# Kernel optimization log

Measured on AMD Instinct MI355X. Metric: run time of the kernel, lower is better.

The kernel has to match this reference:

```python
import jax, jax.numpy as jnp
import numpy as np

NUM_ENTS = 100000
NUM_RELS = 237
IN_CH, OUT_CH, KER = 1, 32, 9
IN_DIM = 200
K = 10
OUT_DIM = K * IN_DIM                      # 2000
L_IN = OUT_DIM // IN_CH                   # 2000
L_OUT = (L_IN - KER) // 1 + 1             # 1992
FC_LEN = OUT_CH * L_OUT                   # 63744
BATCH = 512
EPS = 1e-5


def _bn(x, gamma, beta, axes):
    # training-mode batch norm (biased variance), matching torch BatchNorm1d forward
    m = jnp.mean(x, axis=axes, keepdims=True)
    v = jnp.var(x, axis=axes, keepdims=True)
    return (x - m) * jax.lax.rsqrt(v + EPS) * gamma + beta


def setup_inputs() -> dict:
    key = jax.random.key(0)
    ks = jax.random.split(key, 8)
    xavier = lambda k, shape, fan: jax.random.normal(k, shape, jnp.float32) * np.sqrt(2.0 / fan)
    E = xavier(ks[0], (NUM_ENTS, IN_DIM), NUM_ENTS + IN_DIM)
    R = xavier(ks[1], (NUM_RELS * 2, OUT_CH, IN_CH, KER), OUT_CH * IN_CH * KER)
    e_W = xavier(ks[2], (IN_DIM, OUT_DIM), IN_DIM + OUT_DIM)
    fc_W = xavier(ks[3], (IN_DIM, FC_LEN), IN_DIM + FC_LEN)  # torch Linear weight [out, in]
    return {
        "E": E, "R": R, "e_W": e_W, "fc_W": fc_W,
        "bn0_gamma": jnp.ones((IN_DIM,), jnp.float32), "bn0_beta": jnp.zeros((IN_DIM,), jnp.float32),
        "bn1_gamma": jnp.ones((OUT_CH,), jnp.float32), "bn1_beta": jnp.zeros((OUT_CH,), jnp.float32),
        "bn2_gamma": jnp.ones((IN_DIM,), jnp.float32), "bn2_beta": jnp.zeros((IN_DIM,), jnp.float32),
        "e1_idx": jax.random.randint(ks[4], (BATCH,), 0, NUM_ENTS),
        "r_idx": jax.random.randint(ks[5], (BATCH,), 0, NUM_RELS * 2),
    }


def reference(E, R, e_W, fc_W, bn0_gamma, bn0_beta, bn1_gamma, bn1_beta,
              bn2_gamma, bn2_beta, e1_idx, r_idx):
    B = e1_idx.shape[0]
    x = E[e1_idx]                                   # [B, 200]
    x = _bn(x, bn0_gamma, bn0_beta, axes=0)
    x = x @ e_W                                     # [B, 2000]
    k = R[r_idx]                                    # [B, O, C, KER] per-sample filters
    x = x.reshape(B, IN_CH, L_IN)                   # [B, C, L_in]
    # per-sample grouped conv1d == batched small matmul over sliding windows
    win = jnp.arange(L_OUT)[:, None] + jnp.arange(KER)[None, :]  # [L_out, KER]
    patches = x[:, :, win]                          # [B, C, L_out, KER]
    x = jnp.einsum('bock,bclk->bol', k, patches)    # [B, O, L_out]
    x = _bn(x, bn1_gamma[:, None], bn1_beta[:, None], axes=(0, 2))
    x = x.reshape(B, FC_LEN)
    x = x @ fc_W.T                                  # [B, 200]
    x = jnp.tanh(_bn(x, bn2_gamma, bn2_beta, axes=0))
    logits = x @ E.T                                # [B, num_ents]
    return jax.nn.sigmoid(logits)
```

## Files before the change

kernel.cpp:

```cpp
#include <hip/hip_runtime.h>

#define NENT 100000
#define DIM 200
#define ODIM 2000
#define KERN 9
#define OCH 32
#define LOUT 1992
#define FCLEN 63744
#define BSZ 512
#define EPSV 1e-5f
#define KPAD 224
#define NZ 64

typedef float f32x4 __attribute__((ext_vector_type(4)));
typedef short short8 __attribute__((ext_vector_type(8)));
typedef __bf16 bf16x8 __attribute__((ext_vector_type(8)));
typedef unsigned int uint4v __attribute__((ext_vector_type(4)));
typedef unsigned int uint2v __attribute__((ext_vector_type(2)));

__device__ __forceinline__ unsigned short f2bf(float f) {
  unsigned int u = __float_as_uint(f);
  return (unsigned short)((u + 0x7fffu + ((u >> 16) & 1u)) >> 16);
}

__device__ __forceinline__ float wredf(float v) {
#pragma unroll
  for (int o = 32; o > 0; o >>= 1) v += __shfl_down(v, o, 64);
  return v;
}

__global__ void k_init(float* bias) {
  int t = threadIdx.x;
  if (t < DIM) bias[t] = 0.f;
}

__global__ void k_bn0(const float* __restrict__ E, const int* __restrict__ e1,
                      const float* __restrict__ g, const float* __restrict__ b,
                      float* __restrict__ A, float* __restrict__ Bc) {
  int f = blockIdx.x, ln = threadIdx.x;
  float s1 = 0.f, s2 = 0.f;
  for (int i = ln; i < BSZ; i += 64) {
    float v = E[(long)e1[i] * DIM + f];
    s1 += v; s2 += v * v;
  }
  s1 = wredf(s1); s2 = wredf(s2);
  if (ln == 0) {
    float m = s1 / BSZ;
    float var = s2 / BSZ - m * m;
    float a = g[f] * rsqrtf(var + EPSV);
    A[f] = a; Bc[f] = b[f] - m * a;
  }
}

__global__ void __launch_bounds__(256) k_mm1(
    const float* __restrict__ E, const int* __restrict__ e1,
    const float* __restrict__ eW, const float* __restrict__ A,
    const float* __restrict__ Bc, float* __restrict__ x1) {
  __shared__ float xs[16][DIM];
  int t = threadIdx.x;
  int b0 = blockIdx.x * 16, n0 = blockIdx.y * 128;
  for (int idx = t; idx < 16 * DIM; idx += 256) {
    int bi = idx / DIM, f = idx % DIM;
    xs[bi][f] = E[(long)e1[b0 + bi] * DIM + f] * A[f] + Bc[f];
  }
  __syncthreads();
  int lane = t & 63, w = t >> 6;
  int j0 = n0 + lane, j1 = j0 + 64;
  int r0 = w * 4;
  bool c0 = (j0 < ODIM), c1 = (j1 < ODIM);
  float acc[4][2];
#pragma unroll
  for (int r = 0; r < 4; r++) { acc[r][0] = 0.f; acc[r][1] = 0.f; }
  for (int k = 0; k < DIM; k += 4) {
    f32x4 xr[4];
#pragma unroll
    for (int r = 0; r < 4; r++) xr[r] = *(const f32x4*)&xs[r0 + r][k];
#pragma unroll
    for (int kk = 0; kk < 4; kk++) {
      float e0v = c0 ? eW[(long)(k + kk) * ODIM + j0] : 0.f;
      float e1v = c1 ? eW[(long)(k + kk) * ODIM + j1] : 0.f;
#pragma unroll
      for (int r = 0; r < 4; r++) {
        acc[r][0] += xr[r][kk] * e0v;
        acc[r][1] += xr[r][kk] * e1v;
      }
    }
  }
#pragma unroll
  for (int r = 0; r < 4; r++) {
    long base = (long)(b0 + r0 + r) * ODIM;
    if (c0) x1[base + j0] = acc[r][0];
    if (c1) x1[base + j1] = acc[r][1];
  }
}

__global__ void __launch_bounds__(256) k_conv(
    const float* __restrict__ x1, const float* __restrict__ R,
    const int* __restrict__ ridx, unsigned short* __restrict__ convb,
    float* __restrict__ part) {
  __shared__ float xs[ODIM];
  __shared__ float kr[OCH * KERN];
  __shared__ float wr4[4][64];
  int t = threadIdx.x, b = blockIdx.x;
  for (int i = t; i < ODIM; i += 256) xs[i] = x1[(long)b * ODIM + i];
  for (int i = t; i < OCH * KERN; i += 256) kr[i] = R[(long)ridx[b] * (OCH * KERN) + i];
  __syncthreads();
  int l0 = t * 8;
  bool act = (t < 249);
  float w[16];
  if (act) {
#pragma unroll
    for (int i = 0; i < 16; i++) w[i] = xs[l0 + i];
  }
  int wv = t >> 6, ln = t & 63;
  for (int o = 0; o < OCH; o++) {
    float s1 = 0.f, s2 = 0.f;
    if (act) {
      float kk[KERN];
#pragma unroll
      for (int k = 0; k < KERN; k++) kk[k] = kr[o * KERN + k];
      float cb[8];
#pragma unroll
      for (int j = 0; j < 8; j++) {
        float c = 0.f;
#pragma unroll
        for (int k = 0; k < KERN; k++) c += kk[k] * w[j + k];
        cb[j] = c; s1 += c; s2 += c * c;
      }
      uint4v pk;
#pragma unroll
      for (int i = 0; i < 4; i++)
        pk[i] = (unsigned)f2bf(cb[2 * i]) | ((unsigned)f2bf(cb[2 * i + 1]) << 16);
      *(uint4v*)(convb + (long)b * FCLEN + o * LOUT + l0) = pk;
    }
    s1 = wredf(s1); s2 = wredf(s2);
    if (ln == 0) { wr4[wv][o] = s1; wr4[wv][o + 32] = s2; }
  }
  __syncthreads();
  if (t < 64) part[(long)b * 64 + t] = wr4[0][t] + wr4[1][t] + wr4[2][t] + wr4[3][t];
}

__global__ void k_bn1fin(const float* __restrict__ part, const float* __restrict__ g,
                         const float* __restrict__ b, float* __restrict__ a,
                         float* __restrict__ c) {
  __shared__ float sm[4][64];
  __shared__ float tot[64];
  int t = threadIdx.x;
  int si = t >> 6, st = t & 63;
  float s = 0.f;
  for (int i = si; i < BSZ; i += 4) s += part[(long)i * 64 + st];
  sm[si][st] = s;
  __syncthreads();
  if (t < 64) tot[t] = sm[0][t] + sm[1][t] + sm[2][t] + sm[3][t];
  __syncthreads();
  if (t < OCH) {
    float N = (float)BSZ * LOUT;
    float m = tot[t] / N;
    float var = tot[t + 32] / N - m * m;
    float av = g[t] * rsqrtf(var + EPSV);
    a[t] = av; c[t] = b[t] - m * av;
  }
}

__global__ void __launch_bounds__(256) k_fcw(
    const float* __restrict__ fcW, const float* __restrict__ a,
    const float* __restrict__ c, unsigned short* __restrict__ fcWb,
    float* __restrict__ bias) {
  int d = blockIdx.x, o = blockIdx.y, t = threadIdx.x;
  const float* src = fcW + (long)d * FCLEN + o * LOUT;
  unsigned short* dst = fcWb + (long)d * FCLEN + o * LOUT;
  float ao = a[o];
  float s = 0.f;
  if (t < 249) {
    float v[8];
#pragma unroll
    for (int j = 0; j < 8; j++) { v[j] = src[t * 8 + j]; s += v[j]; }
    uint4v pk;
#pragma unroll
    for (int i = 0; i < 4; i++)
      pk[i] = (unsigned)f2bf(v[2 * i] * ao) | ((unsigned)f2bf(v[2 * i + 1] * ao) << 16);
    *(uint4v*)(dst + t * 8) = pk;
  }
  s = wredf(s);
  __shared__ float sm[4];
  if ((t & 63) == 0) sm[t >> 6] = s;
  __syncthreads();
  if (t == 0) atomicAdd(bias + d, c[o] * (sm[0] + sm[1] + sm[2] + sm[3]));
}

__global__ void __launch_bounds__(256) k_gemm_fc(
    const unsigned short* __restrict__ convb, const unsigned short* __restrict__ fcWb,
    float* __restrict__ ypart) {
  __shared__ unsigned short lA[128 * 104];
  __shared__ unsigned short lB[128 * 104];
  int t = threadIdx.x;
  int b0 = blockIdx.x * 128, n0 = blockIdx.y * 128, z = blockIdx.z;
  int s0 = (664 * z) / NZ, s1 = (664 * (z + 1)) / NZ;
  int w = t >> 6, lane = t & 63, lm = lane & 15, quad = lane >> 4;
  int mq = (w >> 1) * 64, nq = (w & 1) * 64;
  f32x4 acc[4][4];
#pragma unroll
  for (int mi = 0; mi < 4; mi++)
#pragma unroll
    for (int ni = 0; ni < 4; ni++) acc[mi][ni] = (f32x4){0.f, 0.f, 0.f, 0.f};
  for (int st = s0; st < s1; st++) {
    long kc = (long)st * 96;
    __syncthreads();
#pragma unroll
    for (int i = 0; i < 6; i++) {
      int cc = t + 256 * i;
      int row = cc / 12, c8 = cc % 12;
      *(uint4v*)&lA[row * 104 + c8 * 8] =
          *(const uint4v*)&convb[(long)(b0 + row) * FCLEN + kc + c8 * 8];
      uint4v bv = (uint4v){0u, 0u, 0u, 0u};
      int nr = n0 + row;
      if (nr < DIM) bv = *(const uint4v*)&fcWb[(long)nr * FCLEN + kc + c8 * 8];
      *(uint4v*)&lB[row * 104 + c8 * 8] = bv;
    }
    __syncthreads();
#pragma unroll
    for (int ks = 0; ks < 96; ks += 32) {
      short8 af[4], bfr[4];
#pragma unroll
      for (int i2 = 0; i2 < 4; i2++) {
        af[i2] = *(const short8*)&lA[(mq + i2 * 16 + lm) * 104 + ks + quad * 8];
        bfr[i2] = *(const short8*)&lB[(nq + i2 * 16 + lm) * 104 + ks + quad * 8];
      }
#pragma unroll
      for (int mi = 0; mi < 4; mi++)
#pragma unroll
        for (int ni = 0; ni < 4; ni++)
          acc[mi][ni] = __builtin_amdgcn_mfma_f32_16x16x32_bf16(
              __builtin_bit_cast(bf16x8, af[mi]), __builtin_bit_cast(bf16x8, bfr[ni]),
              acc[mi][ni], 0, 0, 0);
    }
  }
#pragma unroll
  for (int mi = 0; mi < 4; mi++)
#pragma unroll
    for (int ni = 0; ni < 4; ni++)
#pragma unroll
      for (int r = 0; r < 4; r++) {
        int gm = b0 + mq + mi * 16 + quad * 4 + r;
        int gn = n0 + nq + ni * 16 + lm;
        ypart[((long)z * BSZ + gm) * 256 + gn] = acc[mi][ni][r];
      }
}

__global__ void __launch_bounds__(256) k_yred(
    const float* __restrict__ ypart, const float* __restrict__ bias,
    float* __restrict__ y) {
  int i = blockIdx.x * 256 + threadIdx.x;
  int m = i / DIM, d = i % DIM;
  float s = bias[d];
#pragma unroll 8
  for (int z = 0; z < NZ; z++) s += ypart[((long)z * BSZ + m) * 256 + d];
  y[(long)m * DIM + d] = s;
}

__global__ void k_bn2(const float* __restrict__ y, const float* __restrict__ g,
                      const float* __restrict__ b, unsigned short* __restrict__ xt) {
  int d = blockIdx.x, ln = threadIdx.x;
  if (d >= DIM) {
    for (int i = ln; i < BSZ; i += 64) xt[(long)i * KPAD + d] = 0;
    return;
  }
  float v[8];
  float s1 = 0.f, s2 = 0.f;
#pragma unroll
  for (int j = 0; j < 8; j++) {
    v[j] = y[(long)(ln + 64 * j) * DIM + d];
    s1 += v[j]; s2 += v[j] * v[j];
  }
  s1 = wredf(s1); s2 = wredf(s2);
  s1 = __shfl(s1, 0, 64); s2 = __shfl(s2, 0, 64);
  float m = s1 / BSZ, var = s2 / BSZ - m * m;
  float a = g[d] * rsqrtf(var + EPSV), c = b[d] - m * a;
#pragma unroll
  for (int j = 0; j < 8; j++)
    xt[(long)(ln + 64 * j) * KPAD + d] = f2bf(tanhf(v[j] * a + c));
}

__global__ void __launch_bounds__(256, 3) k_gemmf(
    const unsigned short* __restrict__ xt, const float* __restrict__ E,
    float* __restrict__ out) {
  __shared__ unsigned short lB[64 * 232];
  int t = threadIdx.x;
  long e0 = (long)blockIdx.x * 64;
  int m0 = blockIdx.y * 256;
#pragma unroll
  for (int i = 0; i < 13; i++) {
    int cc = t + 256 * i;
    if (cc < 3200) {
      int row = cc / 50, c4 = cc % 50;
      long e = e0 + row;
      f32x4 v = (f32x4){0.f, 0.f, 0.f, 0.f};
      if (e < NENT) v = *(const f32x4*)&E[e * DIM + c4 * 4];
      uint2v pk;
      pk[0] = (unsigned)f2bf(v[0]) | ((unsigned)f2bf(v[1]) << 16);
      pk[1] = (unsigned)f2bf(v[2]) | ((unsigned)f2bf(v[3]) << 16);
      *(uint2v*)&lB[row * 232 + c4 * 4] = pk;
    }
  }
  {
    int row = t >> 2, cp = t & 3;
    uint4v zz = (uint4v){0u, 0u, 0u, 0u};
    *(uint4v*)&lB[row * 232 + 200 + cp * 8] = zz;
  }
  __syncthreads();
  int w = t >> 6, lane = t & 63, lm = lane & 15, quad = lane >> 4;
  int r0 = m0 + w * 64;
  f32x4 acc[4][4];
#pragma unroll
  for (int mi = 0; mi < 4; mi++)
#pragma unroll
    for (int ni = 0; ni < 4; ni++) acc[mi][ni] = (f32x4){0.f, 0.f, 0.f, 0.f};
#pragma unroll
  for (int kk = 0; kk < 7; kk++) {
    int k0 = kk * 32;
    short8 bfr[4];
#pragma unroll
    for (int ni = 0; ni < 4; ni++)
      bfr[ni] = *(const short8*)&lB[(ni * 16 + lm) * 232 + k0 + quad * 8];
#pragma unroll
    for (int mi = 0; mi < 4; mi++) {
      short8 af = *(const short8*)&xt[(long)(r0 + mi * 16 + lm) * KPAD + k0 + quad * 8];
#pragma unroll
      for (int ni = 0; ni < 4; ni++)
        acc[mi][ni] = __builtin_amdgcn_mfma_f32_16x16x32_bf16(
            __builtin_bit_cast(bf16x8, af), __builtin_bit_cast(bf16x8, bfr[ni]),
            acc[mi][ni], 0, 0, 0);
    }
  }
#pragma unroll
  for (int mi = 0; mi < 4; mi++)
#pragma unroll
    for (int ni = 0; ni < 4; ni++)
#pragma unroll
      for (int r = 0; r < 4; r++) {
        int gb = r0 + mi * 16 + quad * 4 + r;
        long ge = e0 + ni * 16 + lm;
        if (ge < NENT) {
          float x = acc[mi][ni][r];
          float sg = 1.f / (1.f + __expf(-x));
          __builtin_nontemporal_store(sg, &out[(long)gb * NENT + ge]);
        }
      }
}

extern "C" void kernel_launch(void* const* d_in, const int* in_sizes, int n_in,
                              void* d_out, int out_size, void* d_ws, size_t ws_size,
                              hipStream_t stream) {
  const float* E = (const float*)d_in[0];
  const float* R = (const float*)d_in[1];
  const float* eW = (const float*)d_in[2];
  const float* fcW = (const float*)d_in[3];
  const float* bn0g = (const float*)d_in[4];
  const float* bn0b = (const float*)d_in[5];
  const float* bn1g = (const float*)d_in[6];
  const float* bn1b = (const float*)d_in[7];
  const float* bn2g = (const float*)d_in[8];
  const float* bn2b = (const float*)d_in[9];
  const int* e1 = (const int*)d_in[10];
  const int* ridx = (const int*)d_in[11];
  float* outp = (float*)d_out;

  char* p = (char*)d_ws;
  size_t off = 0;
  auto alloc = [&](size_t bytes) -> char* {
    char* r = p + off;
    off = (off + bytes + 255) & ~(size_t)255;
    return r;
  };
  float* x1 = (float*)alloc((size_t)BSZ * ODIM * 4);
  unsigned short* convb = (unsigned short*)alloc((size_t)BSZ * FCLEN * 2);
  unsigned short* fcWb = (unsigned short*)alloc((size_t)DIM * FCLEN * 2);
  float* ypart = (float*)alloc((size_t)NZ * BSZ * 256 * 4);
  float* y = (float*)alloc((size_t)BSZ * DIM * 4);
  unsigned short* xt = (unsigned short*)alloc((size_t)BSZ * KPAD * 2);
  float* bn0A = (float*)alloc(DIM * 4);
  float* bn0B = (float*)alloc(DIM * 4);
  float* part = (float*)alloc((size_t)BSZ * 64 * 4);
  float* bn1a = (float*)alloc(OCH * 4);
  float* bn1c = (float*)alloc(OCH * 4);
  float* bias = (float*)alloc(DIM * 4);

  k_init<<<1, 256, 0, stream>>>(bias);
  k_bn0<<<DIM, 64, 0, stream>>>(E, e1, bn0g, bn0b, bn0A, bn0B);
  k_mm1<<<dim3(32, 16), 256, 0, stream>>>(E, e1, eW, bn0A, bn0B, x1);
  k_conv<<<BSZ, 256, 0, stream>>>(x1, R, ridx, convb, part);
  k_bn1fin<<<1, 256, 0, stream>>>(part, bn1g, bn1b, bn1a, bn1c);
  k_fcw<<<dim3(DIM, OCH), 256, 0, stream>>>(fcW, bn1a, bn1c, fcWb, bias);
  k_gemm_fc<<<dim3(4, 2, NZ), 256, 0, stream>>>(convb, fcWb, ypart);
  k_yred<<<400, 256, 0, stream>>>(ypart, bias, y);
  k_bn2<<<KPAD, 64, 0, stream>>>(y, bn2g, bn2b, xt);
  k_gemmf<<<dim3((NENT + 63) / 64, 2), 256, 0, stream>>>(xt, E, outp);
}
```

Measured before the change: 548.7 us.

## Pre-convert E to padded bf16 and drop LDS staging in final GEMM

Adds a separate kernel that converts the entity table E to a padded bf16 copy once per call. The final logits GEMM then reads bf16 fragments straight from global memory instead of staging fp32-to-bf16 conversions in LDS. The grid is retiled so each wave covers 64 entities by 64 batch rows, with 8 batch tiles. This removes per-block LDS fills and barriers and halves the bytes of E that each tile reads. The cost is an extra full pass over E (read fp32, write bf16), and E is now reread 8 times from global/L2 rather than twice. The nontemporal output store is also replaced by a plain store.

New measurement: 572.0 us. 1.04x slower.

```diff
diff --git a/kernel.cpp b/kernel.cpp
--- a/kernel.cpp
+++ b/kernel.cpp
@@ -11,6 +11,7 @@
 #define EPSV 1e-5f
 #define KPAD 224
 #define NZ 64
+#define EROWS 100096
 
 typedef float f32x4 __attribute__((ext_vector_type(4)));
 typedef short short8 __attribute__((ext_vector_type(8)));
@@ -32,6 +33,18 @@
 __global__ void k_init(float* bias) {
   int t = threadIdx.x;
   if (t < DIM) bias[t] = 0.f;
+}
+
+__global__ void __launch_bounds__(256) k_ebf(const float* __restrict__ E,
+                                             unsigned short* __restrict__ Ebf) {
+  long idx = (long)blockIdx.x * 256 + threadIdx.x;
+  int row = (int)(idx / 56), c4 = (int)(idx % 56);
+  f32x4 v = (f32x4){0.f, 0.f, 0.f, 0.f};
+  if (row < NENT && c4 < 50) v = *(const f32x4*)&E[(long)row * DIM + c4 * 4];
+  uint2v pk;
+  pk[0] = (unsigned)f2bf(v[0]) | ((unsigned)f2bf(v[1]) << 16);
+  pk[1] = (unsigned)f2bf(v[2]) | ((unsigned)f2bf(v[3]) << 16);
+  *(uint2v*)&Ebf[(long)row * KPAD + c4 * 4] = pk;
 }
 
 __global__ void k_bn0(const float* __restrict__ E, const int* __restrict__ e1,
@@ -281,56 +294,34 @@
     xt[(long)(ln + 64 * j) * KPAD + d] = f2bf(tanhf(v[j] * a + c));
 }
 
-__global__ void __launch_bounds__(256, 3) k_gemmf(
-    const unsigned short* __restrict__ xt, const float* __restrict__ E,
+__global__ void __launch_bounds__(256, 4) k_gemmf(
+    const unsigned short* __restrict__ xt, const unsigned short* __restrict__ Ebf,
     float* __restrict__ out) {
-  __shared__ unsigned short lB[64 * 232];
-  int t = threadIdx.x;
-  long e0 = (long)blockIdx.x * 64;
-  int m0 = blockIdx.y * 256;
-#pragma unroll
-  for (int i = 0; i < 13; i++) {
-    int cc = t + 256 * i;
-    if (cc < 3200) {
-      int row = cc / 50, c4 = cc % 50;
-      long e = e0 + row;
-      f32x4 v = (f32x4){0.f, 0.f, 0.f, 0.f};
-      if (e < NENT) v = *(const f32x4*)&E[e * DIM + c4 * 4];
-      uint2v pk;
-      pk[0] = (unsigned)f2bf(v[0]) | ((unsigned)f2bf(v[1]) << 16);
-      pk[1] = (unsigned)f2bf(v[2]) | ((unsigned)f2bf(v[3]) << 16);
-      *(uint2v*)&lB[row * 232 + c4 * 4] = pk;
-    }
-  }
-  {
-    int row = t >> 2, cp = t & 3;
-    uint4v zz = (uint4v){0u, 0u, 0u, 0u};
-    *(uint4v*)&lB[row * 232 + 200 + cp * 8] = zz;
-  }
-  __syncthreads();
+  int t = threadIdx.x;
   int w = t >> 6, lane = t & 63, lm = lane & 15, quad = lane >> 4;
-  int r0 = m0 + w * 64;
+  long ew = (long)blockIdx.x * 256 + w * 64;
+  int m0 = blockIdx.y * 64;
   f32x4 acc[4][4];
 #pragma unroll
   for (int mi = 0; mi < 4; mi++)
 #pragma unroll
     for (int ni = 0; ni < 4; ni++) acc[mi][ni] = (f32x4){0.f, 0.f, 0.f, 0.f};
-#pragma unroll
   for (int kk = 0; kk < 7; kk++) {
     int k0 = kk * 32;
-    short8 bfr[4];
+    short8 bfr[4], af[4];
 #pragma unroll
     for (int ni = 0; ni < 4; ni++)
-      bfr[ni] = *(const short8*)&lB[(ni * 16 + lm) * 232 + k0 + quad * 8];
-#pragma unroll
-    for (int mi = 0; mi < 4; mi++) {
-      short8 af = *(const short8*)&xt[(long)(r0 + mi * 16 + lm) * KPAD + k0 + quad * 8];
+      bfr[ni] = *(const short8*)&Ebf[(ew + ni * 16 + lm) * KPAD + k0 + quad * 8];
+#pragma unroll
+    for (int mi = 0; mi < 4; mi++)
+      af[mi] = *(const short8*)&xt[(long)(m0 + mi * 16 + lm) * KPAD + k0 + quad * 8];
+#pragma unroll
+    for (int mi = 0; mi < 4; mi++)
 #pragma unroll
       for (int ni = 0; ni < 4; ni++)
         acc[mi][ni] = __builtin_amdgcn_mfma_f32_16x16x32_bf16(
-            __builtin_bit_cast(bf16x8, af), __builtin_bit_cast(bf16x8, bfr[ni]),
+            __builtin_bit_cast(bf16x8, af[mi]), __builtin_bit_cast(bf16x8, bfr[ni]),
             acc[mi][ni], 0, 0, 0);
-    }
   }
 #pragma unroll
   for (int mi = 0; mi < 4; mi++)
@@ -338,12 +329,11 @@
     for (int ni = 0; ni < 4; ni++)
 #pragma unroll
       for (int r = 0; r < 4; r++) {
-        int gb = r0 + mi * 16 + quad * 4 + r;
-        long ge = e0 + ni * 16 + lm;
+        int gb = m0 + mi * 16 + quad * 4 + r;
+        long ge = ew + ni * 16 + lm;
         if (ge < NENT) {
           float x = acc[mi][ni][r];
-          float sg = 1.f / (1.f + __expf(-x));
-          __builtin_nontemporal_store(sg, &out[(long)gb * NENT + ge]);
+          out[(long)gb * NENT + ge] = 1.f / (1.f + __expf(-x));
         }
       }
 }
@@ -375,6 +365,7 @@
   float* x1 = (float*)alloc((size_t)BSZ * ODIM * 4);
   unsigned short* convb = (unsigned short*)alloc((size_t)BSZ * FCLEN * 2);
   unsigned short* fcWb = (unsigned short*)alloc((size_t)DIM * FCLEN * 2);
+  unsigned short* Ebf = (unsigned short*)alloc((size_t)EROWS * KPAD * 2);
   float* ypart = (float*)alloc((size_t)NZ * BSZ * 256 * 4);
   float* y = (float*)alloc((size_t)BSZ * DIM * 4);
   unsigned short* xt = (unsigned short*)alloc((size_t)BSZ * KPAD * 2);
@@ -386,6 +377,7 @@
   float* bias = (float*)alloc(DIM * 4);
 
   k_init<<<1, 256, 0, stream>>>(bias);
+  k_ebf<<<(EROWS * 56) / 256, 256, 0, stream>>>(E, Ebf);
   k_bn0<<<DIM, 64, 0, stream>>>(E, e1, bn0g, bn0b, bn0A, bn0B);
   k_mm1<<<dim3(32, 16), 256, 0, stream>>>(E, e1, eW, bn0A, bn0B, x1);
   k_conv<<<BSZ, 256, 0, stream>>>(x1, R, ridx, convb, part);
@@ -394,5 +386,5 @@
   k_gemm_fc<<<dim3(4, 2, NZ), 256, 0, stream>>>(convb, fcWb, ypart);
   k_yred<<<400, 256, 0, stream>>>(ypart, bias, y);
   k_bn2<<<KPAD, 64, 0, stream>>>(y, bn2g, bn2b, xt);
-  k_gemmf<<<dim3((NENT + 63) / 64, 2), 256, 0, stream>>>(xt, E, outp);
-}
+  k_gemmf<<<dim3(391, 8), 256, 0, stream>>>(xt, Ebf, outp);
+}
```
